# Performance work log

Hardware: AMD Instinct MI355X
Metric: run time of the kernel (lower is better)

The kernel has to match this reference:

```python
import jax, jax.numpy as jnp
import numpy as np

# Module hyperparameters (from init_kwargs)
M = 2049          # NpointsMesh (odd)
TAU = 3e-6        # Gaussian spreading width
XLIMS = (0.0, 1.0)
MU0 = 1.0
L = abs(XLIMS[1] - XLIMS[0])
TWO_PI = 2.0 * np.pi
B, N = 16, 512


def _grids():
    kGrid = jnp.asarray(np.linspace(-(M // 2), M // 2, M), jnp.float32)
    xGrid = jnp.asarray(TWO_PI * np.linspace(XLIMS[0], XLIMS[1], M + 1)[:-1] / L, jnp.float32)
    return kGrid, xGrid


def setup_inputs() -> dict:
    key = jax.random.key(0)
    kx, = jax.random.split(key, 1)
    x = jax.random.uniform(kx, (B, N), dtype=jnp.float32)  # points inside xLims
    kGrid, _ = _grids()
    multRe0 = (4.0 * np.pi / (kGrid ** 2 + MU0 ** 2))[None, :].astype(jnp.float32)
    multRe1 = (4.0 * np.pi / (kGrid ** 2 + 1.0))[None, :].astype(jnp.float32)
    zeros = jnp.zeros((1, M), jnp.float32)
    return {"x": x, "multRe0": multRe0, "multIm0": zeros,
            "multRe1": multRe1, "multIm1": zeros}


def reference(x, multRe0, multIm0, multRe1, multIm1):
    kGrid, xGrid = _grids()
    # Gaussian spreading: (B, N, M)
    diff = x[..., None] * (TWO_PI / L) - xGrid
    g = jnp.exp(-(diff * diff) / (4.0 * TAU))
    red = jnp.sum(g, axis=1)  # (B, M)
    # NOTE: tf.signal.fftshift/ifftshift default to ALL axes; jnp matches that default.
    fftG = jnp.fft.fftshift(jnp.fft.fft(jax.lax.complex(red, jnp.zeros_like(red)))) * (L / TWO_PI)
    deconv = jnp.sqrt(np.pi / TAU) * jnp.exp((kGrid ** 2) * TAU)  # (M,) real
    rfft = fftG * deconv
    Re, Im = jnp.real(rfft), jnp.imag(rfft)

    def mix(mRe, mIm):
        # Faithful to source (incl. its naming quirk): real = mRe*Re - mRe*Im,
        # imag = mIm*Re + mIm*Im
        return jax.lax.complex(mRe * Re - mRe * Im, mIm * Re + mIm * Im)

    multFFT = jnp.stack([mix(multRe0, multIm0), mix(multRe1, multIm1)], axis=1)  # (B, 2, M)
    multDeconv = multFFT * deconv  # broadcast over (B, 2, M)
    irfft = jnp.real(jnp.fft.ifft(jnp.fft.ifftshift(multDeconv)))  # (B, 2, M)
    # local = irfft[:,None,:,:] * g[:,:,None,:]; fmm = sum over mesh / M  -> einsum
    fmm = jnp.einsum('bnm,bcm->bnc', g, irfft) / M  # (B, N, 2)
    return fmm
```

## Files before the change

### kernel.cpp

```cpp
#include <hip/hip_runtime.h>
#include <math.h>

#define MM 2049
#define BB 16
#define NN 512
#define JH 1025
#define JP 1040
#define SZ 8
#define PCH 128
#define JCH 5
#define TB 16
#define JS 16
#define JSL 65
#define NTC 65

static constexpr double D_TWO_PI    = 6.283185307179586476925286766559;
static constexpr double D_STEP      = D_TWO_PI / 2049.0;
static constexpr float  F_TWO_PI    = 6.28318530717958647692f;
static constexpr float  INV_4TAU    = 83333.33333333333f;
static constexpr float  PI_OVER_TAU = 1047197.5511965977f;
static constexpr float  TWO_TAU     = 6.0e-6f;
static constexpr float  INV_2PI     = 0.15915494309189533f;
static constexpr float  INV_M       = 1.0f / 2049.0f;
static constexpr float  WINF        = 8.0f;


__global__ void k_sdft1(const float* __restrict__ x, float2* __restrict__ PSp,
                        float* __restrict__ out) {
    __shared__ float  LA[PCH];
    __shared__ float  LB[PCH];
    __shared__ float2 SD[PCH];
    __shared__ float  Lz;
    const int b  = blockIdx.y;
    const int z  = blockIdx.z;
    const int a0 = 1 + PCH * z;
    const int b0 = 2049 - PCH * (z + 1);
    if (blockIdx.x == 0 && z == 0) {
        for (int i = threadIdx.x; i < NN * 2; i += 256) out[b * NN * 2 + i] = 0.0f;
    }
    for (int i = threadIdx.x; i < PCH; i += 256) { LA[i] = 0.0f; LB[i] = 0.0f; }
    if (threadIdx.x == 0) Lz = 0.0f;
    __syncthreads();
    for (int n = threadIdx.x; n < NN; n += 256) {
        float xv = x[b * NN + n];
        float xa = xv * F_TWO_PI;
        float p  = xv * (float)MM;
        int m0 = (int)ceilf(p - WINF);  if (m0 < 0) m0 = 0;
        int m1 = (int)floorf(p + WINF); if (m1 > MM - 1) m1 = MM - 1;
        bool hitA = (m1 >= a0) && (m0 <= a0 + PCH - 1);
        bool hitB = (m1 >= b0) && (m0 <= b0 + PCH - 1);
        bool hit0 = (z == 0) && (m0 == 0);
        if (!(hitA || hitB || hit0)) continue;
        for (int m = m0; m <= m1; ++m) {
            float xg = (float)((double)m * D_STEP);
            float d  = xa - xg;
            float g  = expf(-(d * d) * INV_4TAU);
            unsigned ia = (unsigned)(m - a0);
            unsigned ib = (unsigned)(m - b0);
            if (ia < PCH) atomicAdd(&LA[ia], g);
            if (ib < PCH) atomicAdd(&LB[ib], g);
            if (hit0 && m == 0) atomicAdd(&Lz, g);
        }
    }
    __syncthreads();
    for (int i = threadIdx.x; i < PCH; i += 256) {
        float ra = LA[i], rb = LB[PCH - 1 - i];
        SD[i] = make_float2(ra + rb, ra - rb);
    }
    __syncthreads();
    const int j = blockIdx.x * 256 + threadIdx.x;
    if (j >= JH) return;
    float ct, st;
    { float ang = (float)((double)j * D_STEP); __sincosf(ang, &st, &ct); }
    float c, s;
    { int r0 = (j * a0) % MM; float ph = (float)((double)r0 * D_STEP); __sincosf(ph, &s, &c); }
    float accc = 0.0f, accs = 0.0f;
    #pragma unroll 4
    for (int i = 0; i < PCH; ++i) {
        float2 sd = SD[i];
        accc = fmaf(sd.x, c, accc);
        accs = fmaf(sd.y, s, accs);
        float t1 = s * st, t2 = s * ct;
        float cn = fmaf(c, ct, -t1);
        float sn = fmaf(c, st,  t2);
        c = cn; s = sn;
    }
    if (z == 0) accc += Lz;
    PSp[((size_t)b * SZ + z) * JP + j] = make_float2(accc, accs);
}

__global__ __launch_bounds__(256)
void k_dft2g(const float2* __restrict__ PSp,
             const float* __restrict__ mRe0, const float* __restrict__ mIm0,
             const float* __restrict__ mRe1, const float* __restrict__ mIm1,
             const float* __restrict__ x, float* __restrict__ out) {
    __shared__ float4 lab[JH];
    __shared__ float2 irfL[TB];
    __shared__ float2 irfH[TB];
    const int tc  = blockIdx.x;
    const int b   = blockIdx.y;
    const int t0  = tc * TB;
    const int tid = threadIdx.x;

    for (int i = tid; i < JH; i += 256) {
        const int j = i;
        float cs = 0.0f, sn = 0.0f;
        const float2* base = PSp + (size_t)b * SZ * JP + j;
        #pragma unroll
        for (int z = 0; z < SZ; ++z) {
            float2 ps = base[(size_t)z * JP];
            cs += ps.x; sn += ps.y;
        }
        const int msh = j + 1024;
        const float jf = (float)j;
        const float d2 = PI_OVER_TAU * expf(jf * jf * TWO_TAU);
        const float fac = (j == 0) ? 1.0f : 2.0f;
        const float sc = INV_2PI * d2 * fac;
        float4 v;
        v.x =  sc * mRe1[msh] * cs;
        v.y =  sc * mRe0[msh] * cs;
        v.z = -sc * mIm1[msh] * sn;
        v.w = -sc * mIm0[msh] * sn;
        lab[i] = v;
    }
    __syncthreads();

    {
        const int q  = tid & (JS - 1);
        const int tt = tid >> 4;
        const int t  = t0 + tt;
        const int j0 = q * JSL;
        const int j1 = min(j0 + JSL, JH);
        float ct, st;
        { float ang = (float)((double)t * D_STEP); __sincosf(ang, &st, &ct); }
        float c, s;
        { int r0 = (t * j0) % MM; float ph = (float)((double)r0 * D_STEP); __sincosf(ph, &s, &c); }
        float E0 = 0.0f, O0 = 0.0f, E1 = 0.0f, O1 = 0.0f;
        #pragma unroll 4
        for (int i = j0; i < j1; ++i) {
            float4 v = lab[i];
            E0 = fmaf(v.x, c, E0);
            O0 = fmaf(v.z, s, O0);
            E1 = fmaf(v.y, c, E1);
            O1 = fmaf(v.w, s, O1);
            float t1 = s * st, t2 = s * ct;
            float cn = fmaf(c, ct, -t1);
            float sn2 = fmaf(c, st,  t2);
            c = cn; s = sn2;
        }
        #pragma unroll
        for (int off = 8; off > 0; off >>= 1) {
            E0 += __shfl_xor(E0, off);
            O0 += __shfl_xor(O0, off);
            E1 += __shfl_xor(E1, off);
            O1 += __shfl_xor(O1, off);
        }
        if (q == 0 && t < JH) {
            irfL[tt] = make_float2((E0 - O0) * INV_M, (E1 - O1) * INV_M);
            irfH[tt] = make_float2((E0 + O0) * INV_M, (E1 + O1) * INV_M);
        }
    }
    __syncthreads();

    const int L1 = min(t0 + TB, JH) - 1;
    const int L0 = t0;
    const int H0 = MM - L1, H1 = MM - max(t0, 1);
    for (int n = tid; n < NN; n += 256) {
        const int p = b * NN + n;
        float xv = x[p];
        float xa = xv * F_TWO_PI;
        float pp = xv * (float)MM;
        int m0 = (int)ceilf(pp - WINF);  if (m0 < 0) m0 = 0;
        int m1 = (int)floorf(pp + WINF); if (m1 > MM - 1) m1 = MM - 1;
        float a0 = 0.0f, a1 = 0.0f;
        int lo = max(m0, L0), hi = min(m1, L1);
        for (int m = lo; m <= hi; ++m) {
            float xg = (float)((double)m * D_STEP);
            float d  = xa - xg;
            float g  = expf(-(d * d) * INV_4TAU);
            float2 v = irfL[m - L0];
            a0 = fmaf(g, v.x, a0);
            a1 = fmaf(g, v.y, a1);
        }
        int lo2 = max(m0, H0), hi2 = min(m1, H1);
        for (int m = lo2; m <= hi2; ++m) {
            float xg = (float)((double)m * D_STEP);
            float d  = xa - xg;
            float g  = expf(-(d * d) * INV_4TAU);
            float2 v = irfH[(MM - m) - t0];
            a0 = fmaf(g, v.x, a0);
            a1 = fmaf(g, v.y, a1);
        }
        if ((hi >= lo) || (hi2 >= lo2)) {
            atomicAdd(&out[p * 2 + 0], a0 * INV_M);
            atomicAdd(&out[p * 2 + 1], a1 * INV_M);
        }
    }
}

extern "C" void kernel_launch(void* const* d_in, const int* in_sizes, int n_in,
                              void* d_out, int out_size, void* d_ws, size_t ws_size,
                              hipStream_t stream) {
    const float* x    = (const float*)d_in[0];
    const float* mRe0 = (const float*)d_in[1];
    const float* mIm0 = (const float*)d_in[2];
    const float* mRe1 = (const float*)d_in[3];
    const float* mIm1 = (const float*)d_in[4];
    float* out = (float*)d_out;

    float2* PSp = (float2*)d_ws;

    k_sdft1<<<dim3(JCH, BB, SZ), 256, 0, stream>>>(x, PSp, out);
    k_dft2g<<<dim3(NTC, BB), 256, 0, stream>>>(PSp, mRe0, mIm0, mRe1, mIm1, x, out);
}
```

Baseline: 91.01 us.

## Compute two output frequencies per thread in the inverse DFT stage

Each thread in the second kernel now evaluates two output indices, reusing each shared-memory load of the spectrum for both, and the number of output tiles per batch is halved. This cuts redundant rebuilding of the shared spectrum table per block (fewer blocks) and halves LDS reads per FMA. The trade-off is more registers per thread and fewer blocks to fill the GPU (33x16 instead of 65x16).

```diff
diff --git a/kernel.cpp b/kernel.cpp
--- a/kernel.cpp
+++ b/kernel.cpp
@@ -9,10 +9,10 @@
 #define SZ 8
 #define PCH 128
 #define JCH 5
-#define TB 16
+#define TB 32
 #define JS 16
 #define JSL 65
-#define NTC 65
+#define NTC 33
 
 static constexpr double D_TWO_PI    = 6.283185307179586476925286766559;
 static constexpr double D_STEP      = D_TWO_PI / 2049.0;
@@ -128,42 +128,64 @@
     {
         const int q  = tid & (JS - 1);
         const int tt = tid >> 4;
-        const int t  = t0 + tt;
+        const int tA = t0 + tt;
+        const int tB = t0 + JS + tt;
         const int j0 = q * JSL;
         const int j1 = min(j0 + JSL, JH);
-        float ct, st;
-        { float ang = (float)((double)t * D_STEP); __sincosf(ang, &st, &ct); }
-        float c, s;
-        { int r0 = (t * j0) % MM; float ph = (float)((double)r0 * D_STEP); __sincosf(ph, &s, &c); }
-        float E0 = 0.0f, O0 = 0.0f, E1 = 0.0f, O1 = 0.0f;
+        float ctA, stA, ctB, stB;
+        { float a = (float)((double)tA * D_STEP); __sincosf(a, &stA, &ctA); }
+        { float a = (float)((double)tB * D_STEP); __sincosf(a, &stB, &ctB); }
+        float cA, sA, cB, sB;
+        { int r0 = (tA * j0) % MM; float ph = (float)((double)r0 * D_STEP); __sincosf(ph, &sA, &cA); }
+        { int r0 = (tB * j0) % MM; float ph = (float)((double)r0 * D_STEP); __sincosf(ph, &sB, &cB); }
+        float EA0 = 0.0f, OA0 = 0.0f, EA1 = 0.0f, OA1 = 0.0f;
+        float EB0 = 0.0f, OB0 = 0.0f, EB1 = 0.0f, OB1 = 0.0f;
         #pragma unroll 4
         for (int i = j0; i < j1; ++i) {
             float4 v = lab[i];
-            E0 = fmaf(v.x, c, E0);
-            O0 = fmaf(v.z, s, O0);
-            E1 = fmaf(v.y, c, E1);
-            O1 = fmaf(v.w, s, O1);
-            float t1 = s * st, t2 = s * ct;
-            float cn = fmaf(c, ct, -t1);
-            float sn2 = fmaf(c, st,  t2);
-            c = cn; s = sn2;
+            EA0 = fmaf(v.x, cA, EA0);
+            OA0 = fmaf(v.z, sA, OA0);
+            EA1 = fmaf(v.y, cA, EA1);
+            OA1 = fmaf(v.w, sA, OA1);
+            EB0 = fmaf(v.x, cB, EB0);
+            OB0 = fmaf(v.z, sB, OB0);
+            EB1 = fmaf(v.y, cB, EB1);
+            OB1 = fmaf(v.w, sB, OB1);
+            { float t1 = sA * stA, t2 = sA * ctA;
+              float cn = fmaf(cA, ctA, -t1);
+              float sn = fmaf(cA, stA,  t2);
+              cA = cn; sA = sn; }
+            { float t1 = sB * stB, t2 = sB * ctB;
+              float cn = fmaf(cB, ctB, -t1);
+              float sn = fmaf(cB, stB,  t2);
+              cB = cn; sB = sn; }
         }
         #pragma unroll
         for (int off = 8; off > 0; off >>= 1) {
-            E0 += __shfl_xor(E0, off);
-            O0 += __shfl_xor(O0, off);
-            E1 += __shfl_xor(E1, off);
-            O1 += __shfl_xor(O1, off);
-        }
-        if (q == 0 && t < JH) {
-            irfL[tt] = make_float2((E0 - O0) * INV_M, (E1 - O1) * INV_M);
-            irfH[tt] = make_float2((E0 + O0) * INV_M, (E1 + O1) * INV_M);
-        }
-    }
-    __syncthreads();
-
+            EA0 += __shfl_xor(EA0, off);
+            OA0 += __shfl_xor(OA0, off);
+            EA1 += __shfl_xor(EA1, off);
+            OA1 += __shfl_xor(OA1, off);
+            EB0 += __shfl_xor(EB0, off);
+            OB0 += __shfl_xor(OB0, off);
+            EB1 += __shfl_xor(EB1, off);
+            OB1 += __shfl_xor(OB1, off);
+        }
+        if (q == 0) {
+            if (tA < JH) {
+                irfL[tt] = make_float2((EA0 - OA0) * INV_M, (EA1 - OA1) * INV_M);
+                irfH[tt] = make_float2((EA0 + OA0) * INV_M, (EA1 + OA1) * INV_M);
+            }
+            if (tB < JH) {
+                irfL[JS + tt] = make_float2((EB0 - OB0) * INV_M, (EB1 - OB1) * INV_M);
+                irfH[JS + tt] = make_float2((EB0 + OB0) * INV_M, (EB1 + OB1) * INV_M);
+            }
+        }
+    }
+    __syncthreads();
+
+    const int L0 = t0;
     const int L1 = min(t0 + TB, JH) - 1;
-    const int L0 = t0;
     const int H0 = MM - L1, H1 = MM - max(t0, 1);
     for (int n = tid; n < NN; n += 256) {
         const int p = b * NN + n;
```

Result: no change. 92.05 us, median of 2 (+1.1%).
